# Performance work log

Hardware: AMD Instinct MI355X
Metric: run time of the kernel (lower is better)

Reference implementation:

```python
import jax, jax.numpy as jnp
import numpy as np
import math

B, T, C, H = 4, 4096, 512, 64  # batch, seq_len, n_embed, head_size


def setup_inputs() -> dict:
    key = jax.random.key(0)
    kx, kq, kk, kv = jax.random.split(key, 4)
    scale = 1.0 / math.sqrt(C)  # ~Linear init scale
    return {
        "x": jax.random.normal(kx, (B, T, C), dtype=jnp.float32),
        "Wq": jax.random.normal(kq, (C, H), dtype=jnp.float32) * scale,
        "Wk": jax.random.normal(kk, (C, H), dtype=jnp.float32) * scale,
        "Wv": jax.random.normal(kv, (C, H), dtype=jnp.float32) * scale,
    }


def reference(x, Wq, Wk, Wv):
    # Single-head causal self-attention (mask=True path, dropout=0/eval).
    # NOTE: original module scales by 1/sqrt(C) (n_embed), not 1/sqrt(head_size).
    Bn, Tn, Cn = x.shape
    q = x @ Wq  # [B,T,H]
    k = x @ Wk  # [B,T,H]
    v = x @ Wv  # [B,T,H]
    inv_scale = jnp.float32(1.0 / math.sqrt(Cn))
    scores = jnp.einsum('bth,bsh->bts', q, k) * inv_scale  # [B,T,T]
    causal = jnp.tril(jnp.ones((Tn, Tn), dtype=bool))
    scores = jnp.where(causal, scores, jnp.float32(-jnp.inf))
    attn = jax.nn.softmax(scores, axis=-1)
    out = jnp.einsum('bts,bsh->bth', attn, v)  # [B,T,H]
    return out
```

## Files before the change

### kernel.cpp

```cpp
#include <hip/hip_runtime.h>
#include <math.h>

#define BATCH 4
#define SEQT  4096
#define CDIM  512
#define HDIM  64

typedef unsigned short ushort_t;
typedef __attribute__((ext_vector_type(8))) short bf16x8;
typedef __attribute__((ext_vector_type(4))) float f32x4;

#define MFMA16(a, b, c) __builtin_amdgcn_mfma_f32_16x16x32_bf16((a), (b), (c), 0, 0, 0)
#define NEG (-1e30f)

__device__ __forceinline__ ushort_t f2bf(float f) {
  union { float f; unsigned int u; } v;
  v.f = f;
  unsigned int u = v.u;
  u += 0x7fffu + ((u >> 16) & 1u);
  return (ushort_t)(u >> 16);
}
__device__ __forceinline__ unsigned int pk2(float a, float b) {
  return (unsigned int)f2bf(a) | ((unsigned int)f2bf(b) << 16);
}

__global__ __launch_bounds__(256) void convert_w(
    const float* __restrict__ Wq, const float* __restrict__ Wk,
    const float* __restrict__ Wv, ushort_t* __restrict__ wtf) {
  int g = blockIdx.x * 256 + threadIdx.x;
  int lane = g & 63;
  int nt = (g >> 6) & 3;
  int ks = (g >> 8) & 15;
  int mat = g >> 12;
  const float* W = (mat == 0) ? Wq : (mat == 1) ? Wk : Wv;
  const float sc = (mat == 0) ? 0.04419417382415922f : 1.0f;
  int n = lane & 15, quad = lane >> 4;
  int h = nt * 16 + n;
  int c0 = ks * 32 + quad * 8;
  ushort_t tmp[8];
#pragma unroll
  for (int j = 0; j < 8; ++j) tmp[j] = f2bf(W[(c0 + j) * HDIM + h] * sc);
  *(bf16x8*)(wtf + (size_t)g * 8) = *(const bf16x8*)tmp;
}

__global__ __launch_bounds__(384) void qkv_proj(
    const float* __restrict__ x, const ushort_t* __restrict__ wtf,
    ushort_t* __restrict__ qbf, ushort_t* __restrict__ kbf,
    ushort_t* __restrict__ vbf) {
  __shared__ ushort_t Xs[16 * 512];
  __shared__ float Facc[3 * 1088];
  __shared__ ushort_t Pk[3][16 * 64];

  const int tid = threadIdx.x;
  const int row0 = blockIdx.x * 16;

  const float4* xg = (const float4*)(x + (size_t)row0 * CDIM);
  for (int i = tid; i < 16 * (CDIM / 4); i += 384) {
    float4 xv = xg[i];
    int r = i >> 7, c4 = i & 127;
    int chunk = (c4 >> 1) ^ (r & 7);
    uint2 u;
    u.x = pk2(xv.x, xv.y);
    u.y = pk2(xv.z, xv.w);
    *(uint2*)&Xs[r * 512 + chunk * 8 + (c4 & 1) * 4] = u;
  }
  __syncthreads();

  const int lane = tid & 63;
  const int w = tid >> 6;
  const int mat = w >> 1;
  const int kh = w & 1;
  const int n = lane & 15, quad = lane >> 4;
  const ushort_t* wb = wtf + mat * 32768;

  f32x4 acc[4];
#pragma unroll
  for (int nt = 0; nt < 4; ++nt) acc[nt] = (f32x4){0.f, 0.f, 0.f, 0.f};

  bf16x8 bcur[4];
#pragma unroll
  for (int nt = 0; nt < 4; ++nt)
    bcur[nt] = *(const bf16x8*)&wb[(kh * 8 * 4 + nt) * 512 + lane * 8];

  for (int kk = 0; kk < 8; ++kk) {
    const int ks = kh * 8 + kk;
    bf16x8 a = *(const bf16x8*)&Xs[n * 512 + ((4 * ks + quad) ^ (n & 7)) * 8];
    bf16x8 bnext[4];
    if (kk < 7) {
#pragma unroll
      for (int nt = 0; nt < 4; ++nt)
        bnext[nt] = *(const bf16x8*)&wb[((ks + 1) * 4 + nt) * 512 + lane * 8];
    }
#pragma unroll
    for (int nt = 0; nt < 4; ++nt) acc[nt] = MFMA16(a, bcur[nt], acc[nt]);
    if (kk < 7) {
#pragma unroll
      for (int nt = 0; nt < 4; ++nt) bcur[nt] = bnext[nt];
    }
  }

  if (kh == 1) {
#pragma unroll
    for (int nt = 0; nt < 4; ++nt)
#pragma unroll
      for (int i = 0; i < 4; ++i)
        Facc[mat * 1088 + lane * 17 + nt * 4 + i] = acc[nt][i];
  }
  __syncthreads();

  if (kh == 0) {
#pragma unroll
    for (int nt = 0; nt < 4; ++nt)
#pragma unroll
      for (int i = 0; i < 4; ++i) {
        acc[nt][i] += Facc[mat * 1088 + lane * 17 + nt * 4 + i];
        const int row = quad * 4 + i;
        Pk[mat][row * 64 + (((2 * nt + (n >> 3)) ^ (row & 7)) * 8) + (n & 7)] =
            f2bf(acc[nt][i]);
      }
    if (mat < 2) {
      ushort_t* dst = (mat == 0) ? qbf : kbf;
#pragma unroll
      for (int ks2 = 0; ks2 < 2; ++ks2) {
        bf16x8 fr = *(const bf16x8*)&Pk[mat][n * 64 +
                                            (((4 * ks2 + quad) ^ (n & 7)) * 8)];
        *(bf16x8*)(dst + (size_t)((row0 >> 4) * 2 + ks2) * 512 + lane * 8) = fr;
      }
    } else {
      const int b = row0 >> 12, t0 = row0 & 4095;
      const int kt = t0 >> 6, kslot = (t0 >> 5) & 1, tsub = (t0 >> 4) & 1;
      if ((quad >> 1) == tsub) {
        const int lq = quad & 1;
#pragma unroll
        for (int nt = 0; nt < 4; ++nt) {
          ushort_t tmp[8];
#pragma unroll
          for (int j = 0; j < 8; ++j) {
            const int row = lq * 8 + j;
            tmp[j] = Pk[2][row * 64 +
                           (((2 * nt + (n >> 3)) ^ (row & 7)) * 8) + (n & 7)];
          }
          *(bf16x8*)(vbf + (size_t)(((b * 64 + kt) * 4 + nt) * 2 + kslot) * 512 +
                     lane * 8) = *(const bf16x8*)tmp;
        }
      }
    }
  }
}

__global__ __launch_bounds__(512, 4) void attn(
    const ushort_t* __restrict__ qbf, const ushort_t* __restrict__ kbf,
    const ushort_t* __restrict__ vbf, float* __restrict__ out) {
  __shared__ __align__(16) char smem[35328];
  ushort_t* Ps = (ushort_t*)smem;
  float* Om = (float*)smem;
  float* Ol = (float*)(smem + 34816);

  const int tid = threadIdx.x;
  const int lane = tid & 63;
  const int w = tid >> 6;
  const int m2 = w & 1;
  const int kt0 = w >> 1;
  const int n = lane & 15, quad = lane >> 4;

  const int b = blockIdx.x & 3;
  const int qt = 127 - (blockIdx.x >> 2);
  const int q0 = qt * 32;

  const ushort_t* qB = qbf + (size_t)b * 512 * 512;
  const ushort_t* kB = kbf + (size_t)b * 512 * 512;
  const ushort_t* vB = vbf + (size_t)b * 512 * 512;
  float* oB = out + (size_t)b * SEQT * HDIM;

  bf16x8 qf[2];
#pragma unroll
  for (int ks = 0; ks < 2; ++ks)
    qf[ks] = *(const bf16x8*)&qB[(size_t)((qt * 2 + m2) * 2 + ks) * 512 +
                                 lane * 8];

  bf16x8 ones;
#pragma unroll
  for (int j = 0; j < 8; ++j) ones[j] = (short)0x3F80;

  f32x4 o[4], ol;
#pragma unroll
  for (int nt = 0; nt < 4; ++nt) o[nt] = (f32x4){0.f, 0.f, 0.f, 0.f};
  ol = (f32x4){0.f, 0.f, 0.f, 0.f};

  const int ktiles = (q0 + 95) >> 6;
  ushort_t* Pw = Ps + w * 1024;

  for (int kt = kt0; kt < ktiles; kt += 4) {
    const int k0 = kt * 64;

    f32x4 s[4];
#pragma unroll
    for (int nt = 0; nt < 4; ++nt) s[nt] = (f32x4){0.f, 0.f, 0.f, 0.f};
#pragma unroll
    for (int ks = 0; ks < 2; ++ks)
#pragma unroll
      for (int nt = 0; nt < 4; ++nt) {
        bf16x8 kf = *(const bf16x8*)&kB[(size_t)((kt * 4 + nt) * 2 + ks) * 512 +
                                        lane * 8];
        s[nt] = MFMA16(qf[ks], kf, s[nt]);
      }

    if (k0 + 63 > q0) {
      const int rbase = q0 + m2 * 16 + quad * 4;
#pragma unroll
      for (int nt = 0; nt < 4; ++nt) {
        const int col = k0 + nt * 16 + n;
#pragma unroll
        for (int i = 0; i < 4; ++i)
          if (col > rbase + i) s[nt][i] = NEG;
      }
    }

#pragma unroll
    for (int nt = 0; nt < 4; ++nt)
#pragma unroll
      for (int i = 0; i < 4; ++i) {
        const int row = quad * 4 + i;
        Pw[row * 64 + (((2 * nt + (n >> 3)) ^ (row & 7)) * 8) + (n & 7)] =
            f2bf(__expf(s[nt][i]));
      }

    bf16x8 pa0 = *(const bf16x8*)&Pw[n * 64 + ((quad ^ (n & 7)) * 8)];
    bf16x8 pa1 = *(const bf16x8*)&Pw[n * 64 + (((4 + quad) ^ (n & 7)) * 8)];
    ol = MFMA16(pa0, ones, ol);
    ol = MFMA16(pa1, ones, ol);
#pragma unroll
    for (int nt = 0; nt < 4; ++nt) {
      bf16x8 vf = *(const bf16x8*)&vB[(size_t)((kt * 4 + nt) * 2 + 0) * 512 +
                                      lane * 8];
      o[nt] = MFMA16(pa0, vf, o[nt]);
    }
#pragma unroll
    for (int nt = 0; nt < 4; ++nt) {
      bf16x8 vf = *(const bf16x8*)&vB[(size_t)((kt * 4 + nt) * 2 + 1) * 512 +
                                      lane * 8];
      o[nt] = MFMA16(pa1, vf, o[nt]);
    }
  }

  __syncthreads();

  float* OmW = Om + w * 1088;
#pragma unroll
  for (int nt = 0; nt < 4; ++nt)
#pragma unroll
    for (int i = 0; i < 4; ++i)
      OmW[(quad * 4 + i) * 68 + nt * 16 + n] = o[nt][i];
  if (n == 0)
#pragma unroll
    for (int i = 0; i < 4; ++i) Ol[w * 16 + quad * 4 + i] = ol[i];
  __syncthreads();

  {
    const int r = tid >> 4;
    const int c0 = (tid & 15) * 4;
    const int m2r = r >> 4, lr = r & 15;
    float ax = 0.f, ay = 0.f, az = 0.f, aw = 0.f, ls = 0.f;
#pragma unroll
    for (int ww = 0; ww < 4; ++ww) {
      const int wi = m2r + ww * 2;
      const float4 vv = *(const float4*)&Om[wi * 1088 + lr * 68 + c0];
      ax += vv.x; ay += vv.y; az += vv.z; aw += vv.w;
      ls += Ol[wi * 16 + lr];
    }
    const float inv = 1.0f / ls;
    *(float4*)&oB[(size_t)(q0 + r) * HDIM + c0] =
        make_float4(ax * inv, ay * inv, az * inv, aw * inv);
  }
}

extern "C" void kernel_launch(void* const* d_in, const int* in_sizes, int n_in,
                              void* d_out, int out_size, void* d_ws, size_t ws_size,
                              hipStream_t stream) {
  const float* x = (const float*)d_in[0];
  const float* Wq = (const float*)d_in[1];
  const float* Wk = (const float*)d_in[2];
  const float* Wv = (const float*)d_in[3];
  float* out = (float*)d_out;

  ushort_t* wtf = (ushort_t*)d_ws;
  ushort_t* qbf = wtf + 3 * 16 * 4 * 512;
  ushort_t* kbf = qbf + (size_t)BATCH * 512 * 512;
  ushort_t* vbf = kbf + (size_t)BATCH * 512 * 512;

  convert_w<<<48, 256, 0, stream>>>(Wq, Wk, Wv, wtf);
  qkv_proj<<<BATCH * SEQT / 16, 384, 0, stream>>>(x, wtf, qbf, kbf, vbf);
  attn<<<512, 512, 0, stream>>>(qbf, kbf, vbf, out);
}
```

Baseline: 129.9 us.

## Have each wave process both query row-tiles over split key tiles

Each wave now computes both 16-row query sub-tiles of the 32-row block, so every loaded K and V fragment feeds two MFMAs and the keys are split across all 8 waves instead of 4. The row sum of probabilities is accumulated in fp32 registers and reduced with lane shuffles, replacing the MFMA-against-ones trick. The cost is double the accumulator registers, twice the shared memory (about 70KB per block, which may limit blocks per CU), and an 8-way cross-wave reduction at the end.

```diff
diff --git a/kernel.cpp b/kernel.cpp
--- a/kernel.cpp
+++ b/kernel.cpp
@@ -151,16 +151,14 @@
 __global__ __launch_bounds__(512, 4) void attn(
     const ushort_t* __restrict__ qbf, const ushort_t* __restrict__ kbf,
     const ushort_t* __restrict__ vbf, float* __restrict__ out) {
-  __shared__ __align__(16) char smem[35328];
+  __shared__ __align__(16) char smem[70656];
   ushort_t* Ps = (ushort_t*)smem;
   float* Om = (float*)smem;
-  float* Ol = (float*)(smem + 34816);
+  float* Ol = (float*)(smem + 69632);
 
   const int tid = threadIdx.x;
   const int lane = tid & 63;
   const int w = tid >> 6;
-  const int m2 = w & 1;
-  const int kt0 = w >> 1;
   const int n = lane & 15, quad = lane >> 4;
 
   const int b = blockIdx.x & 3;
@@ -172,101 +170,126 @@
   const ushort_t* vB = vbf + (size_t)b * 512 * 512;
   float* oB = out + (size_t)b * SEQT * HDIM;
 
-  bf16x8 qf[2];
-#pragma unroll
-  for (int ks = 0; ks < 2; ++ks)
-    qf[ks] = *(const bf16x8*)&qB[(size_t)((qt * 2 + m2) * 2 + ks) * 512 +
-                                 lane * 8];
-
-  bf16x8 ones;
-#pragma unroll
-  for (int j = 0; j < 8; ++j) ones[j] = (short)0x3F80;
-
-  f32x4 o[4], ol;
-#pragma unroll
-  for (int nt = 0; nt < 4; ++nt) o[nt] = (f32x4){0.f, 0.f, 0.f, 0.f};
-  ol = (f32x4){0.f, 0.f, 0.f, 0.f};
+  bf16x8 qf[2][2];
+#pragma unroll
+  for (int m2 = 0; m2 < 2; ++m2)
+#pragma unroll
+    for (int ks = 0; ks < 2; ++ks)
+      qf[m2][ks] = *(const bf16x8*)&qB[(size_t)((qt * 2 + m2) * 2 + ks) * 512 +
+                                       lane * 8];
+
+  f32x4 o[2][4];
+  float lsum[2][4];
+#pragma unroll
+  for (int m2 = 0; m2 < 2; ++m2)
+#pragma unroll
+    for (int nt = 0; nt < 4; ++nt) o[m2][nt] = (f32x4){0.f, 0.f, 0.f, 0.f};
+#pragma unroll
+  for (int m2 = 0; m2 < 2; ++m2)
+#pragma unroll
+    for (int i = 0; i < 4; ++i) lsum[m2][i] = 0.f;
 
   const int ktiles = (q0 + 95) >> 6;
-  ushort_t* Pw = Ps + w * 1024;
-
-  for (int kt = kt0; kt < ktiles; kt += 4) {
+  ushort_t* Pw = Ps + w * 2048;
+
+  for (int kt = w; kt < ktiles; kt += 8) {
     const int k0 = kt * 64;
 
-    f32x4 s[4];
-#pragma unroll
-    for (int nt = 0; nt < 4; ++nt) s[nt] = (f32x4){0.f, 0.f, 0.f, 0.f};
+    f32x4 s[2][4];
+#pragma unroll
+    for (int m2 = 0; m2 < 2; ++m2)
+#pragma unroll
+      for (int nt = 0; nt < 4; ++nt) s[m2][nt] = (f32x4){0.f, 0.f, 0.f, 0.f};
 #pragma unroll
     for (int ks = 0; ks < 2; ++ks)
 #pragma unroll
       for (int nt = 0; nt < 4; ++nt) {
         bf16x8 kf = *(const bf16x8*)&kB[(size_t)((kt * 4 + nt) * 2 + ks) * 512 +
                                         lane * 8];
-        s[nt] = MFMA16(qf[ks], kf, s[nt]);
+        s[0][nt] = MFMA16(qf[0][ks], kf, s[0][nt]);
+        s[1][nt] = MFMA16(qf[1][ks], kf, s[1][nt]);
       }
 
     if (k0 + 63 > q0) {
-      const int rbase = q0 + m2 * 16 + quad * 4;
+#pragma unroll
+      for (int m2 = 0; m2 < 2; ++m2) {
+        const int rbase = q0 + m2 * 16 + quad * 4;
+#pragma unroll
+        for (int nt = 0; nt < 4; ++nt) {
+          const int col = k0 + nt * 16 + n;
+#pragma unroll
+          for (int i = 0; i < 4; ++i)
+            if (col > rbase + i) s[m2][nt][i] = NEG;
+        }
+      }
+    }
+
+#pragma unroll
+    for (int m2 = 0; m2 < 2; ++m2)
+#pragma unroll
+      for (int nt = 0; nt < 4; ++nt)
+#pragma unroll
+        for (int i = 0; i < 4; ++i) {
+          const float p = __expf(s[m2][nt][i]);
+          lsum[m2][i] += p;
+          const int row = m2 * 16 + quad * 4 + i;
+          Pw[row * 64 + (((2 * nt + (n >> 3)) ^ (row & 7)) * 8) + (n & 7)] =
+              f2bf(p);
+        }
+
+    bf16x8 pa[2][2];
+#pragma unroll
+    for (int m2 = 0; m2 < 2; ++m2)
+#pragma unroll
+      for (int ks = 0; ks < 2; ++ks)
+        pa[m2][ks] = *(const bf16x8*)&Pw[(m2 * 16 + n) * 64 +
+                                         (((4 * ks + quad) ^ (n & 7)) * 8)];
+#pragma unroll
+    for (int ks = 0; ks < 2; ++ks)
 #pragma unroll
       for (int nt = 0; nt < 4; ++nt) {
-        const int col = k0 + nt * 16 + n;
-#pragma unroll
-        for (int i = 0; i < 4; ++i)
-          if (col > rbase + i) s[nt][i] = NEG;
-      }
-    }
-
+        bf16x8 vf = *(const bf16x8*)&vB[(size_t)((kt * 4 + nt) * 2 + ks) * 512 +
+                                        lane * 8];
+        o[0][nt] = MFMA16(pa[0][ks], vf, o[0][nt]);
+        o[1][nt] = MFMA16(pa[1][ks], vf, o[1][nt]);
+      }
+  }
+
+#pragma unroll
+  for (int off = 1; off < 16; off <<= 1)
+#pragma unroll
+    for (int m2 = 0; m2 < 2; ++m2)
+#pragma unroll
+      for (int i = 0; i < 4; ++i)
+        lsum[m2][i] += __shfl_xor(lsum[m2][i], off);
+
+  __syncthreads();
+
+  float* OmW = Om + w * 2176;
+#pragma unroll
+  for (int m2 = 0; m2 < 2; ++m2)
 #pragma unroll
     for (int nt = 0; nt < 4; ++nt)
 #pragma unroll
-      for (int i = 0; i < 4; ++i) {
-        const int row = quad * 4 + i;
-        Pw[row * 64 + (((2 * nt + (n >> 3)) ^ (row & 7)) * 8) + (n & 7)] =
-            f2bf(__expf(s[nt][i]));
-      }
-
-    bf16x8 pa0 = *(const bf16x8*)&Pw[n * 64 + ((quad ^ (n & 7)) * 8)];
-    bf16x8 pa1 = *(const bf16x8*)&Pw[n * 64 + (((4 + quad) ^ (n & 7)) * 8)];
-    ol = MFMA16(pa0, ones, ol);
-    ol = MFMA16(pa1, ones, ol);
-#pragma unroll
-    for (int nt = 0; nt < 4; ++nt) {
-      bf16x8 vf = *(const bf16x8*)&vB[(size_t)((kt * 4 + nt) * 2 + 0) * 512 +
-                                      lane * 8];
-      o[nt] = MFMA16(pa0, vf, o[nt]);
-    }
-#pragma unroll
-    for (int nt = 0; nt < 4; ++nt) {
-      bf16x8 vf = *(const bf16x8*)&vB[(size_t)((kt * 4 + nt) * 2 + 1) * 512 +
-                                      lane * 8];
-      o[nt] = MFMA16(pa1, vf, o[nt]);
-    }
-  }
-
-  __syncthreads();
-
-  float* OmW = Om + w * 1088;
-#pragma unroll
-  for (int nt = 0; nt < 4; ++nt)
-#pragma unroll
-    for (int i = 0; i < 4; ++i)
-      OmW[(quad * 4 + i) * 68 + nt * 16 + n] = o[nt][i];
+      for (int i = 0; i < 4; ++i)
+        OmW[(m2 * 16 + quad * 4 + i) * 68 + nt * 16 + n] = o[m2][nt][i];
   if (n == 0)
 #pragma unroll
-    for (int i = 0; i < 4; ++i) Ol[w * 16 + quad * 4 + i] = ol[i];
+    for (int m2 = 0; m2 < 2; ++m2)
+#pragma unroll
+      for (int i = 0; i < 4; ++i)
+        Ol[w * 32 + m2 * 16 + quad * 4 + i] = lsum[m2][i];
   __syncthreads();
 
   {
     const int r = tid >> 4;
     const int c0 = (tid & 15) * 4;
-    const int m2r = r >> 4, lr = r & 15;
     float ax = 0.f, ay = 0.f, az = 0.f, aw = 0.f, ls = 0.f;
 #pragma unroll
-    for (int ww = 0; ww < 4; ++ww) {
-      const int wi = m2r + ww * 2;
-      const float4 vv = *(const float4*)&Om[wi * 1088 + lr * 68 + c0];
+    for (int ww = 0; ww < 8; ++ww) {
+      const float4 vv = *(const float4*)&Om[ww * 2176 + r * 68 + c0];
       ax += vv.x; ay += vv.y; az += vv.z; aw += vv.w;
-      ls += Ol[wi * 16 + lr];
+      ls += Ol[ww * 32 + r];
     }
     const float inv = 1.0f / ls;
     *(float4*)&oB[(size_t)(q0 + r) * HDIM + c0] =
```

After: 143.4 us. +10.4%, slower.

## Pair mirrored 16-row query tiles per block and split keys across eight waves

Applied to the files above, without the earlier changes.

Each attention block now handles two 16-row query tiles, one from each end of the sequence, so causal work is balanced across blocks. All eight waves split the key tiles of one query tile instead of two row halves times four key groups. The row sum is now accumulated in registers with shuffles rather than an extra MFMA against a ones vector. The projection kernel also swaps XOR-swizzled LDS layouts for padded row strides. This adds two extra cross-wave reductions and barriers per block, and the per-tile key range is shorter, which may limit overlap.

```diff
diff --git a/kernel.cpp b/kernel.cpp
--- a/kernel.cpp
+++ b/kernel.cpp
@@ -43,13 +43,15 @@
   *(bf16x8*)(wtf + (size_t)g * 8) = *(const bf16x8*)tmp;
 }
 
+#define XP 520
+
 __global__ __launch_bounds__(384) void qkv_proj(
     const float* __restrict__ x, const ushort_t* __restrict__ wtf,
     ushort_t* __restrict__ qbf, ushort_t* __restrict__ kbf,
     ushort_t* __restrict__ vbf) {
-  __shared__ ushort_t Xs[16 * 512];
+  __shared__ ushort_t Xs[16 * XP];
   __shared__ float Facc[3 * 1088];
-  __shared__ ushort_t Pk[3][16 * 64];
+  __shared__ ushort_t Pk[3][16 * 72];
 
   const int tid = threadIdx.x;
   const int row0 = blockIdx.x * 16;
@@ -58,11 +60,10 @@
   for (int i = tid; i < 16 * (CDIM / 4); i += 384) {
     float4 xv = xg[i];
     int r = i >> 7, c4 = i & 127;
-    int chunk = (c4 >> 1) ^ (r & 7);
     uint2 u;
     u.x = pk2(xv.x, xv.y);
     u.y = pk2(xv.z, xv.w);
-    *(uint2*)&Xs[r * 512 + chunk * 8 + (c4 & 1) * 4] = u;
+    *(uint2*)&Xs[r * XP + c4 * 4] = u;
   }
   __syncthreads();
 
@@ -84,7 +85,7 @@
 
   for (int kk = 0; kk < 8; ++kk) {
     const int ks = kh * 8 + kk;
-    bf16x8 a = *(const bf16x8*)&Xs[n * 512 + ((4 * ks + quad) ^ (n & 7)) * 8];
+    bf16x8 a = *(const bf16x8*)&Xs[n * XP + ks * 32 + quad * 8];
     bf16x8 bnext[4];
     if (kk < 7) {
 #pragma unroll
@@ -114,16 +115,14 @@
 #pragma unroll
       for (int i = 0; i < 4; ++i) {
         acc[nt][i] += Facc[mat * 1088 + lane * 17 + nt * 4 + i];
-        const int row = quad * 4 + i;
-        Pk[mat][row * 64 + (((2 * nt + (n >> 3)) ^ (row & 7)) * 8) + (n & 7)] =
-            f2bf(acc[nt][i]);
+        Pk[mat][(quad * 4 + i) * 72 + nt * 16 + n] = f2bf(acc[nt][i]);
       }
     if (mat < 2) {
       ushort_t* dst = (mat == 0) ? qbf : kbf;
 #pragma unroll
       for (int ks2 = 0; ks2 < 2; ++ks2) {
-        bf16x8 fr = *(const bf16x8*)&Pk[mat][n * 64 +
-                                            (((4 * ks2 + quad) ^ (n & 7)) * 8)];
+        bf16x8 fr =
+            *(const bf16x8*)&Pk[mat][n * 72 + ks2 * 32 + quad * 8];
         *(bf16x8*)(dst + (size_t)((row0 >> 4) * 2 + ks2) * 512 + lane * 8) = fr;
       }
     } else {
@@ -135,11 +134,8 @@
         for (int nt = 0; nt < 4; ++nt) {
           ushort_t tmp[8];
 #pragma unroll
-          for (int j = 0; j < 8; ++j) {
-            const int row = lq * 8 + j;
-            tmp[j] = Pk[2][row * 64 +
-                           (((2 * nt + (n >> 3)) ^ (row & 7)) * 8) + (n & 7)];
-          }
+          for (int j = 0; j < 8; ++j)
+            tmp[j] = Pk[2][(lq * 8 + j) * 72 + nt * 16 + n];
           *(bf16x8*)(vbf + (size_t)(((b * 64 + kt) * 4 + nt) * 2 + kslot) * 512 +
                      lane * 8) = *(const bf16x8*)tmp;
         }
@@ -159,118 +155,122 @@
   const int tid = threadIdx.x;
   const int lane = tid & 63;
   const int w = tid >> 6;
-  const int m2 = w & 1;
-  const int kt0 = w >> 1;
   const int n = lane & 15, quad = lane >> 4;
 
   const int b = blockIdx.x & 3;
-  const int qt = 127 - (blockIdx.x >> 2);
-  const int q0 = qt * 32;
+  const int j = blockIdx.x >> 2;
 
   const ushort_t* qB = qbf + (size_t)b * 512 * 512;
   const ushort_t* kB = kbf + (size_t)b * 512 * 512;
   const ushort_t* vB = vbf + (size_t)b * 512 * 512;
   float* oB = out + (size_t)b * SEQT * HDIM;
 
-  bf16x8 qf[2];
-#pragma unroll
-  for (int ks = 0; ks < 2; ++ks)
-    qf[ks] = *(const bf16x8*)&qB[(size_t)((qt * 2 + m2) * 2 + ks) * 512 +
-                                 lane * 8];
-
-  bf16x8 ones;
-#pragma unroll
-  for (int j = 0; j < 8; ++j) ones[j] = (short)0x3F80;
-
-  f32x4 o[4], ol;
-#pragma unroll
-  for (int nt = 0; nt < 4; ++nt) o[nt] = (f32x4){0.f, 0.f, 0.f, 0.f};
-  ol = (f32x4){0.f, 0.f, 0.f, 0.f};
-
-  const int ktiles = (q0 + 95) >> 6;
   ushort_t* Pw = Ps + w * 1024;
 
-  for (int kt = kt0; kt < ktiles; kt += 4) {
-    const int k0 = kt * 64;
-
-    f32x4 s[4];
-#pragma unroll
-    for (int nt = 0; nt < 4; ++nt) s[nt] = (f32x4){0.f, 0.f, 0.f, 0.f};
+#pragma unroll
+  for (int half = 0; half < 2; ++half) {
+    const int qt = half ? j : (255 - j);
+    const int q0 = qt * 16;
+    const int ktiles = (q0 + 79) >> 6;
+
+    bf16x8 qf[2];
 #pragma unroll
     for (int ks = 0; ks < 2; ++ks)
+      qf[ks] = *(const bf16x8*)&qB[(size_t)(qt * 2 + ks) * 512 + lane * 8];
+
+    f32x4 o[4];
+    float lsum[4];
+#pragma unroll
+    for (int nt = 0; nt < 4; ++nt) o[nt] = (f32x4){0.f, 0.f, 0.f, 0.f};
+#pragma unroll
+    for (int i = 0; i < 4; ++i) lsum[i] = 0.f;
+
+    for (int kt = w; kt < ktiles; kt += 8) {
+      const int k0 = kt * 64;
+
+      f32x4 s[4];
+#pragma unroll
+      for (int nt = 0; nt < 4; ++nt) s[nt] = (f32x4){0.f, 0.f, 0.f, 0.f};
+#pragma unroll
+      for (int ks = 0; ks < 2; ++ks)
+#pragma unroll
+        for (int nt = 0; nt < 4; ++nt) {
+          bf16x8 kf = *(const bf16x8*)&kB[(size_t)((kt * 4 + nt) * 2 + ks) * 512 +
+                                          lane * 8];
+          s[nt] = MFMA16(qf[ks], kf, s[nt]);
+        }
+
+      if (k0 + 63 > q0) {
+        const int rbase = q0 + quad * 4;
+#pragma unroll
+        for (int nt = 0; nt < 4; ++nt) {
+          const int col = k0 + nt * 16 + n;
+#pragma unroll
+          for (int i = 0; i < 4; ++i)
+            if (col > rbase + i) s[nt][i] = NEG;
+        }
+      }
+
+#pragma unroll
+      for (int nt = 0; nt < 4; ++nt)
+#pragma unroll
+        for (int i = 0; i < 4; ++i) {
+          const float p = __expf(s[nt][i]);
+          lsum[i] += p;
+          const int row = quad * 4 + i;
+          Pw[row * 64 + (((2 * nt + (n >> 3)) ^ (row & 7)) * 8) + (n & 7)] =
+              f2bf(p);
+        }
+
+      bf16x8 pa0 = *(const bf16x8*)&Pw[n * 64 + ((quad ^ (n & 7)) * 8)];
+      bf16x8 pa1 = *(const bf16x8*)&Pw[n * 64 + (((4 + quad) ^ (n & 7)) * 8)];
 #pragma unroll
       for (int nt = 0; nt < 4; ++nt) {
-        bf16x8 kf = *(const bf16x8*)&kB[(size_t)((kt * 4 + nt) * 2 + ks) * 512 +
+        bf16x8 vf = *(const bf16x8*)&vB[(size_t)((kt * 4 + nt) * 2 + 0) * 512 +
                                         lane * 8];
-        s[nt] = MFMA16(qf[ks], kf, s[nt]);
-      }
-
-    if (k0 + 63 > q0) {
-      const int rbase = q0 + m2 * 16 + quad * 4;
+        o[nt] = MFMA16(pa0, vf, o[nt]);
+      }
 #pragma unroll
       for (int nt = 0; nt < 4; ++nt) {
-        const int col = k0 + nt * 16 + n;
-#pragma unroll
-        for (int i = 0; i < 4; ++i)
-          if (col > rbase + i) s[nt][i] = NEG;
-      }
-    }
-
+        bf16x8 vf = *(const bf16x8*)&vB[(size_t)((kt * 4 + nt) * 2 + 1) * 512 +
+                                        lane * 8];
+        o[nt] = MFMA16(pa1, vf, o[nt]);
+      }
+    }
+
+#pragma unroll
+    for (int off = 1; off < 16; off <<= 1)
+#pragma unroll
+      for (int i = 0; i < 4; ++i) lsum[i] += __shfl_xor(lsum[i], off);
+
+    __syncthreads();
+
+    float* OmW = Om + w * 1088;
 #pragma unroll
     for (int nt = 0; nt < 4; ++nt)
 #pragma unroll
-      for (int i = 0; i < 4; ++i) {
-        const int row = quad * 4 + i;
-        Pw[row * 64 + (((2 * nt + (n >> 3)) ^ (row & 7)) * 8) + (n & 7)] =
-            f2bf(__expf(s[nt][i]));
-      }
-
-    bf16x8 pa0 = *(const bf16x8*)&Pw[n * 64 + ((quad ^ (n & 7)) * 8)];
-    bf16x8 pa1 = *(const bf16x8*)&Pw[n * 64 + (((4 + quad) ^ (n & 7)) * 8)];
-    ol = MFMA16(pa0, ones, ol);
-    ol = MFMA16(pa1, ones, ol);
-#pragma unroll
-    for (int nt = 0; nt < 4; ++nt) {
-      bf16x8 vf = *(const bf16x8*)&vB[(size_t)((kt * 4 + nt) * 2 + 0) * 512 +
-                                      lane * 8];
-      o[nt] = MFMA16(pa0, vf, o[nt]);
-    }
-#pragma unroll
-    for (int nt = 0; nt < 4; ++nt) {
-      bf16x8 vf = *(const bf16x8*)&vB[(size_t)((kt * 4 + nt) * 2 + 1) * 512 +
-                                      lane * 8];
-      o[nt] = MFMA16(pa1, vf, o[nt]);
-    }
-  }
-
-  __syncthreads();
-
-  float* OmW = Om + w * 1088;
-#pragma unroll
-  for (int nt = 0; nt < 4; ++nt)
-#pragma unroll
-    for (int i = 0; i < 4; ++i)
-      OmW[(quad * 4 + i) * 68 + nt * 16 + n] = o[nt][i];
-  if (n == 0)
-#pragma unroll
-    for (int i = 0; i < 4; ++i) Ol[w * 16 + quad * 4 + i] = ol[i];
-  __syncthreads();
-
-  {
-    const int r = tid >> 4;
-    const int c0 = (tid & 15) * 4;
-    const int m2r = r >> 4, lr = r & 15;
-    float ax = 0.f, ay = 0.f, az = 0.f, aw = 0.f, ls = 0.f;
-#pragma unroll
-    for (int ww = 0; ww < 4; ++ww) {
-      const int wi = m2r + ww * 2;
-      const float4 vv = *(const float4*)&Om[wi * 1088 + lr * 68 + c0];
-      ax += vv.x; ay += vv.y; az += vv.z; aw += vv.w;
-      ls += Ol[wi * 16 + lr];
-    }
-    const float inv = 1.0f / ls;
-    *(float4*)&oB[(size_t)(q0 + r) * HDIM + c0] =
-        make_float4(ax * inv, ay * inv, az * inv, aw * inv);
+      for (int i = 0; i < 4; ++i)
+        OmW[(quad * 4 + i) * 68 + nt * 16 + n] = o[nt][i];
+    if (n == 0)
+#pragma unroll
+      for (int i = 0; i < 4; ++i) Ol[w * 16 + quad * 4 + i] = lsum[i];
+    __syncthreads();
+
+    {
+      const int r = tid >> 5;
+      const int c0 = (tid & 31) * 2;
+      float a0 = 0.f, a1 = 0.f, ls = 0.f;
+#pragma unroll
+      for (int ww = 0; ww < 8; ++ww) {
+        a0 += Om[ww * 1088 + r * 68 + c0];
+        a1 += Om[ww * 1088 + r * 68 + c0 + 1];
+        ls += Ol[ww * 16 + r];
+      }
+      const float inv = 1.0f / ls;
+      *(float2*)&oB[(size_t)(q0 + r) * HDIM + c0] =
+          make_float2(a0 * inv, a1 * inv);
+    }
+    __syncthreads();
   }
 }
 
```

New measurement: 119.7 us. 7.8% less time.
